# Optimization experiments

Measured on AMD Instinct MI355X. Metric: run time of the kernel, lower is better.

Reference implementation:

```python
import jax, jax.numpy as jnp
import numpy as np

N, D, H, G = 4096, 256, 4, 16
HEAD_DIM = D // H
LN_EPS = 1e-5
TEMP = 5.0


def setup_inputs() -> dict:
    key = jax.random.key(0)
    ks = jax.random.split(key, 12)
    s = 0.05  # weight init scale
    nrm = lambda k, shp: jax.random.normal(k, shp, jnp.float32) * s
    return {
        "x": jax.random.normal(ks[0], (N, D), jnp.float32),
        "Wq": nrm(ks[1], (D, D)), "bq": jnp.zeros((D,), jnp.float32),
        "Wk": nrm(ks[2], (D, D)), "bk": jnp.zeros((D,), jnp.float32),
        "Wv": nrm(ks[3], (D, D)), "bv": jnp.zeros((D,), jnp.float32),
        "Wv1": nrm(ks[4], (D, D // 2)), "bv1": jnp.zeros((D // 2,), jnp.float32),
        "Wv2": nrm(ks[5], (D // 2, 1)), "bv2": jnp.zeros((1,), jnp.float32),
        "Wc1": nrm(ks[6], (2 * D, D)), "bc1": jnp.zeros((D,), jnp.float32),
        "Wc2": nrm(ks[7], (D, 1)), "bc2": jnp.zeros((1,), jnp.float32),
        "gamma": jnp.ones((D,), jnp.float32),
        "beta": jnp.zeros((D,), jnp.float32),
        "batch": jnp.sort(jax.random.randint(ks[8], (N,), 0, G)),
    }


def reference(x, Wq, bq, Wk, bk, Wv, bv, Wv1, bv1, Wv2, bv2,
              Wc1, bc1, Wc2, bc2, gamma, beta, batch):
    n = x.shape[0]
    # multi-head projections -> [N, H, head_dim]
    Q = (x @ Wq + bq).reshape(n, H, HEAD_DIM)
    K = (x @ Wk + bk).reshape(n, H, HEAD_DIM)
    V = (x @ Wv + bv).reshape(n, H, HEAD_DIM)

    # dense scores [N, N, H], block-diagonal mask by graph membership
    scores = jnp.einsum('nhd,mhd->nmh', Q, K) / np.sqrt(HEAD_DIM).astype(np.float32)
    same_graph = (batch[:, None] == batch[None, :])  # [N, N]
    scores = jnp.where(same_graph[:, :, None], scores, -jnp.inf)
    probs = jax.nn.softmax(scores, axis=1)  # softmax over keys m (dim=1, as in torch)
    # dropout is identity in eval mode
    attended = jnp.einsum('nmh,mhd->nhd', probs, V).reshape(n, D)

    # vulnerability detector MLP: D -> D/2 -> 1, sigmoid
    vuln = jax.nn.sigmoid(jax.nn.relu(x @ Wv1 + bv1) @ Wv2 + bv2)[:, 0]

    # global max pool per graph, broadcast back to nodes
    graph_ctx = jax.ops.segment_max(x, batch, num_segments=G, indices_are_sorted=True)[batch]
    combined = jnp.concatenate([x, graph_ctx], axis=1)  # [N, 2D]
    ctx = jax.nn.sigmoid(jnp.tanh(combined @ Wc1 + bc1) @ Wc2 + bc2)[:, 0]

    mha_avg = probs.mean(axis=(1, 2))  # [N]
    w = 0.6 * vuln + 0.3 * ctx + 0.1 * mha_avg

    # per-graph segment softmax with temperature 5.0
    w5 = w * TEMP
    seg_max = jax.ops.segment_max(w5, batch, num_segments=G, indices_are_sorted=True)[batch]
    e = jnp.exp(w5 - seg_max)
    seg_sum = jax.ops.segment_sum(e, batch, num_segments=G, indices_are_sorted=True)[batch]
    att = e / seg_sum  # [N]

    out = attended * att[:, None] + x  # residual
    # LayerNorm over last dim
    mu = out.mean(axis=-1, keepdims=True)
    var = out.var(axis=-1, keepdims=True)
    out = (out - mu) * jax.lax.rsqrt(var + LN_EPS) * gamma + beta
    return out, att
```

## Files before the change

kernel.cpp:

```cpp
#include <hip/hip_runtime.h>
#include <math.h>

#define N_NODES 4096
#define DIM 256
#define NH 4
#define NG 16
#define LN_EPS 1e-5f
#define TEMP 5.0f
#define RSLACK 4160
#define PS_STRIDE 72
#define QT_MAX 24
#define KC_MAX 6
#define WPG (KC_MAX * QT_MAX * NH)
#define ATTN_UNITS (NG * WPG / 4)

typedef __attribute__((ext_vector_type(8))) short short8;
typedef __attribute__((ext_vector_type(4))) short short4_t;
typedef __attribute__((ext_vector_type(4))) float f32x4;

__device__ __forceinline__ unsigned short f2bf(float f) {
    unsigned u = __builtin_bit_cast(unsigned, f);
    u += 0x7FFFu + ((u >> 16) & 1u);
    return (unsigned short)(u >> 16);
}
__device__ __forceinline__ float bf2f(unsigned short u) {
    return __builtin_bit_cast(float, (unsigned)u << 16);
}
__device__ __forceinline__ float fsigmoid(float z) { return 1.f / (1.f + __expf(-z)); }
__device__ __forceinline__ float ftanh(float z) {
    float t = __expf(2.f * z);
    return (t - 1.f) / (t + 1.f);
}
__device__ __forceinline__ int seg_search(const int* __restrict__ batch, int g) {
    int lo = 0, hi = N_NODES;
    while (lo < hi) {
        int mid = (lo + hi) >> 1;
        if (batch[mid] < g) lo = mid + 1; else hi = mid;
    }
    return lo;
}

__global__ __launch_bounds__(256) void prep_kernel(
    const float* __restrict__ x, const float* __restrict__ Wq,
    const float* __restrict__ Wk, const float* __restrict__ Wv,
    const float* __restrict__ Wv1, const float* __restrict__ Wc1,
    const int* __restrict__ batch,
    unsigned short* __restrict__ xb, unsigned short* __restrict__ WqT,
    unsigned short* __restrict__ WkT, unsigned short* __restrict__ WvT,
    unsigned short* __restrict__ Wv1T, unsigned short* __restrict__ Wc1T,
    float* __restrict__ smax, int* __restrict__ seg) {
    int id = blockIdx.x, tid = threadIdx.x;
    if (id == 1632) {
        if (tid <= NG) seg[tid] = seg_search(batch, tid);
        return;
    }
    if (id >= 1376) {
        int u = id - 1376;
        int gg = u >> 4, c = u & 15;
        int s = seg_search(batch, gg), e = seg_search(batch, gg + 1);
        float mx = -INFINITY;
        for (int i = s + c; i < e; i += 16) mx = fmaxf(mx, x[(size_t)i * DIM + tid]);
        smax[(size_t)u * 256 + tid] = mx;
        return;
    }
    if (id >= 352) {
        int base = (id - 352) * 1024 + tid * 4;
        float4 v = *(const float4*)&x[base];
        short4_t o = {(short)f2bf(v.x), (short)f2bf(v.y), (short)f2bf(v.z), (short)f2bf(v.w)};
        *(short4_t*)&xb[base] = o;
        return;
    }
    const float* src; unsigned short* dst; int K, Nn, tX, rel;
    if (id < 64)       { src = Wq;  dst = WqT;  K = 256; Nn = 256; rel = id;      tX = 8;  }
    else if (id < 128) { src = Wk;  dst = WkT;  K = 256; Nn = 256; rel = id-64;   tX = 8;  }
    else if (id < 192) { src = Wv;  dst = WvT;  K = 256; Nn = 256; rel = id-128;  tX = 8;  }
    else if (id < 224) { src = Wv1; dst = Wv1T; K = 256; Nn = 128; rel = id-192;  tX = 8;  }
    else               { src = Wc1; dst = Wc1T; K = 512; Nn = 256; rel = id-224;  tX = 16; }
    int k0 = (rel % tX) * 32, n0 = (rel / tX) * 32;
    __shared__ float t[32][33];
    int c = tid & 31, r0 = tid >> 5;
#pragma unroll
    for (int p = 0; p < 4; ++p) {
        int rr = p * 8 + r0;
        t[rr][c] = src[(size_t)(k0 + rr) * Nn + n0 + c];
    }
    __syncthreads();
#pragma unroll
    for (int p = 0; p < 4; ++p) {
        int rr = p * 8 + r0;
        dst[(size_t)(n0 + rr) * K + k0 + c] = f2bf(t[c][rr]);
    }
}

__device__ __forceinline__ void gemm_unit(
    int z, int bx, int by,
    const unsigned short* __restrict__ xb,
    const unsigned short* __restrict__ WqT, const unsigned short* __restrict__ WkT,
    const unsigned short* __restrict__ WvT, const unsigned short* __restrict__ Wv1T,
    const unsigned short* __restrict__ Wc1T,
    const float* __restrict__ bq, const float* __restrict__ bk,
    const float* __restrict__ bv, const float* __restrict__ bv1,
    const float* __restrict__ bc1, const float* __restrict__ gcw,
    const float* __restrict__ Wv2, const float* __restrict__ Wc2,
    const int* __restrict__ batch,
    unsigned short* __restrict__ Qb, unsigned short* __restrict__ Kb,
    unsigned short* __restrict__ Vt, float* __restrict__ vacc,
    float* __restrict__ cacc) {
    const unsigned short* WT;
    const float* bias;
    int wstride = 256;
    switch (z) {
        case 0: WT = WqT; bias = bq; break;
        case 1: WT = WkT; bias = bk; break;
        case 2: WT = WvT; bias = bv; break;
        case 3: WT = Wc1T; bias = bc1; wstride = 512; break;
        default: WT = Wv1T; bias = bv1; break;
    }
    int ntn = (z == 4) ? 2 : 4;
    int nt0 = by * ntn;
    int tid = threadIdx.x;
    int w = tid >> 6, lane = tid & 63, m = lane & 15, quad = lane >> 4;
    int bm = bx * 64;
    int rowA = bm + 16 * w + m;
    short8 a[8];
#pragma unroll
    for (int ks = 0; ks < 8; ++ks)
        a[ks] = *(const short8*)&xb[(size_t)rowA * 256 + ks * 32 + quad * 8];
    int node0 = bm + 16 * w + quad * 4;
    int b4[4];
    if (z == 3) {
#pragma unroll
        for (int r = 0; r < 4; ++r) b4[r] = batch[node0 + r];
    }
    for (int nti = 0; nti < ntn; ++nti) {
        int nt = nt0 + nti;
        f32x4 acc = {0.f, 0.f, 0.f, 0.f};
#pragma unroll
        for (int ks = 0; ks < 8; ++ks) {
            short8 b = *(const short8*)&WT[(size_t)(nt * 16 + m) * wstride + ks * 32 + quad * 8];
            acc = __builtin_amdgcn_mfma_f32_16x16x32_bf16(a[ks], b, acc, 0, 0, 0);
        }
        int col = nt * 16 + m;
        float bb = bias[col];
        if (z == 0) {
#pragma unroll
            for (int r = 0; r < 4; ++r) Qb[(size_t)(node0 + r) * 256 + col] = f2bf(acc[r] + bb);
        } else if (z == 1) {
#pragma unroll
            for (int r = 0; r < 4; ++r) Kb[(size_t)(node0 + r) * 256 + col] = f2bf(acc[r] + bb);
        } else if (z == 2) {
            short4_t pk = {(short)f2bf(acc[0] + bb), (short)f2bf(acc[1] + bb),
                           (short)f2bf(acc[2] + bb), (short)f2bf(acc[3] + bb)};
            *(short4_t*)&Vt[(size_t)col * RSLACK + node0] = pk;
        } else if (z == 3) {
            float wc = Wc2[col];
#pragma unroll
            for (int r = 0; r < 4; ++r) {
                float p = ftanh(acc[r] + bb + gcw[b4[r] * 256 + col]) * wc;
#pragma unroll
                for (int mm = 1; mm < 16; mm <<= 1) p += __shfl_xor(p, mm);
                if (m == 0) atomicAdd(&cacc[node0 + r], p);
            }
        } else {
            float wv = Wv2[col];
#pragma unroll
            for (int r = 0; r < 4; ++r) {
                float p = fmaxf(acc[r] + bb, 0.f) * wv;
#pragma unroll
                for (int mm = 1; mm < 16; mm <<= 1) p += __shfl_xor(p, mm);
                if (m == 0) atomicAdd(&vacc[node0 + r], p);
            }
        }
    }
}

__global__ __launch_bounds__(256) void gemm_kernel(
    const unsigned short* __restrict__ xb, const float* __restrict__ smax,
    const float* __restrict__ Wc1,
    const unsigned short* __restrict__ WqT, const unsigned short* __restrict__ WkT,
    const unsigned short* __restrict__ WvT, const unsigned short* __restrict__ Wv1T,
    const unsigned short* __restrict__ Wc1T,
    const float* __restrict__ bq, const float* __restrict__ bk,
    const float* __restrict__ bv, const float* __restrict__ bv1,
    const float* __restrict__ bc1, const float* __restrict__ Wv2,
    const float* __restrict__ Wc2, const int* __restrict__ batch,
    unsigned short* __restrict__ Qb, unsigned short* __restrict__ Kb,
    unsigned short* __restrict__ Vt, float* __restrict__ vacc,
    float* __restrict__ gcw) {
    int tid = threadIdx.x;
    if (blockIdx.x < 16) {
        int g = blockIdx.x;
        __shared__ float gl[256];
        float mx = smax[(size_t)(g * 16) * 256 + tid];
#pragma unroll
        for (int c = 1; c < 16; ++c)
            mx = fmaxf(mx, smax[(size_t)(g * 16 + c) * 256 + tid]);
        gl[tid] = bf2f(f2bf(mx));
        __syncthreads();
        float a0 = 0.f, a1 = 0.f, a2 = 0.f, a3 = 0.f;
        for (int k = 0; k < 256; k += 4) {
            a0 += gl[k + 0] * Wc1[(size_t)(256 + k + 0) * 256 + tid];
            a1 += gl[k + 1] * Wc1[(size_t)(256 + k + 1) * 256 + tid];
            a2 += gl[k + 2] * Wc1[(size_t)(256 + k + 2) * 256 + tid];
            a3 += gl[k + 3] * Wc1[(size_t)(256 + k + 3) * 256 + tid];
        }
        gcw[g * 256 + tid] = (a0 + a1) + (a2 + a3);
        return;
    }
    int u = blockIdx.x - 16;
    int zi = u >> 8;
    int z = (zi == 3) ? 4 : zi;
    int r = u & 255;
    gemm_unit(z, r & 63, r >> 6, xb, WqT, WkT, WvT, Wv1T, Wc1T,
              bq, bk, bv, bv1, bc1, nullptr, Wv2, Wc2, batch,
              Qb, Kb, Vt, vacc, nullptr);
}

__global__ __launch_bounds__(256) void attn_kernel(
    const unsigned short* __restrict__ xb,
    const unsigned short* __restrict__ Qb, const unsigned short* __restrict__ Kb,
    const unsigned short* __restrict__ Vt, const int* __restrict__ seg,
    const unsigned short* __restrict__ Wc1T, const float* __restrict__ bc1,
    const float* __restrict__ gcw, const float* __restrict__ Wc2,
    const int* __restrict__ batch,
    unsigned short* __restrict__ Opart, float* __restrict__ Lpart,
    float* __restrict__ cacc) {
    int tid = threadIdx.x;
    if (blockIdx.x < 256) {
        int r = blockIdx.x;
        gemm_unit(3, r & 63, r >> 6, xb, nullptr, nullptr, nullptr, nullptr, Wc1T,
                  nullptr, nullptr, nullptr, nullptr, bc1, gcw, nullptr, Wc2, batch,
                  nullptr, nullptr, nullptr, nullptr, cacc);
        return;
    }
    __shared__ unsigned short Ps[4 * 16 * PS_STRIDE];
    int w = tid >> 6, lane = tid & 63, m = lane & 15, quad = lane >> 4;
    int wid = (blockIdx.x - 256) * 4 + w;
    int g = wid / WPG;
    int r1 = wid - g * WPG;
    int kc = r1 / (QT_MAX * NH);
    int r2 = r1 - kc * (QT_MAX * NH);
    int qt = r2 >> 2, h = r2 & 3;
    int s = seg[g], e = seg[g + 1];
    int q0 = s + qt * 16;
    int k0 = s + kc * 64;
    if (q0 >= e || k0 >= e) return;

    short8 qa0 = *(const short8*)&Qb[(size_t)(q0 + m) * 256 + h * 64 + quad * 8];
    short8 qa1 = *(const short8*)&Qb[(size_t)(q0 + m) * 256 + h * 64 + 32 + quad * 8];

    f32x4 S[4];
#pragma unroll
    for (int nt = 0; nt < 4; ++nt) {
        int key = k0 + nt * 16 + m;
        short8 kb0 = *(const short8*)&Kb[(size_t)key * 256 + h * 64 + quad * 8];
        short8 kb1 = *(const short8*)&Kb[(size_t)key * 256 + h * 64 + 32 + quad * 8];
        f32x4 sa = {0.f, 0.f, 0.f, 0.f};
        sa = __builtin_amdgcn_mfma_f32_16x16x32_bf16(qa0, kb0, sa, 0, 0, 0);
        sa = __builtin_amdgcn_mfma_f32_16x16x32_bf16(qa1, kb1, sa, 0, 0, 0);
        S[nt] = sa;
    }
    int wbase = w * 16 * PS_STRIDE;
#pragma unroll
    for (int nt = 0; nt < 4; ++nt) {
        bool valid = (k0 + nt * 16 + m) < e;
#pragma unroll
        for (int r = 0; r < 4; ++r) {
            float p = valid ? __expf(S[nt][r] * 0.125f) : 0.f;
            Ps[wbase + (quad * 4 + r) * PS_STRIDE + nt * 16 + m] = f2bf(p);
        }
    }
    __builtin_amdgcn_wave_barrier();
    short8 pa0 = *(const short8*)&Ps[wbase + m * PS_STRIDE + quad * 8];
    short8 pa1 = *(const short8*)&Ps[wbase + m * PS_STRIDE + 32 + quad * 8];

    short8 ones = {16256, 16256, 16256, 16256, 16256, 16256, 16256, 16256};
    f32x4 Lacc = {0.f, 0.f, 0.f, 0.f};
    Lacc = __builtin_amdgcn_mfma_f32_16x16x32_bf16(pa0, ones, Lacc, 0, 0, 0);
    Lacc = __builtin_amdgcn_mfma_f32_16x16x32_bf16(pa1, ones, Lacc, 0, 0, 0);
    f32x4 O[4];
#pragma unroll
    for (int nt = 0; nt < 4; ++nt) {
        const unsigned short* vrow = &Vt[(size_t)(h * 64 + nt * 16 + m) * RSLACK + k0];
        short8 vb0 = *(const short8*)&vrow[quad * 8];
        short8 vb1 = *(const short8*)&vrow[32 + quad * 8];
        f32x4 oa = {0.f, 0.f, 0.f, 0.f};
        oa = __builtin_amdgcn_mfma_f32_16x16x32_bf16(pa0, vb0, oa, 0, 0, 0);
        oa = __builtin_amdgcn_mfma_f32_16x16x32_bf16(pa1, vb1, oa, 0, 0, 0);
        O[nt] = oa;
    }
#pragma unroll
    for (int r = 0; r < 4; ++r) {
        int q = q0 + quad * 4 + r;
        if (q < e) {
            if (m == 0) Lpart[((size_t)kc * N_NODES + q) * 4 + h] = Lacc[r];
#pragma unroll
            for (int nt = 0; nt < 4; ++nt)
                Opart[((size_t)kc * N_NODES + q) * 256 + h * 64 + nt * 16 + m] =
                    f2bf(O[nt][r]);
        }
    }
}

__global__ __launch_bounds__(256) void final_kernel(
    const unsigned short* __restrict__ Opart, const float* __restrict__ Lpart,
    const float* __restrict__ x, const float* __restrict__ vacc,
    const float* __restrict__ cacc, const float* __restrict__ bv2,
    const float* __restrict__ bc2, const float* __restrict__ gamma,
    const float* __restrict__ beta, const int* __restrict__ batch,
    const int* __restrict__ seg, float* __restrict__ out,
    float* __restrict__ att_out) {
    int n = blockIdx.x;
    int tid = threadIdx.x;
    int g = batch[n];
    int s = seg[g], e = seg[g + 1];
    float vb = bv2[0], cb = bc2[0];
    __shared__ float r1[4], r2[4];
    int i1 = s + tid, i2 = s + 256 + tid;
    float w1 = (i1 < e) ? TEMP * (0.6f * fsigmoid(vacc[i1] + vb) +
                                  0.3f * fsigmoid(cacc[i1] + cb) + 0.1f / 4096.f)
                        : -1e30f;
    float w2 = (i2 < e) ? TEMP * (0.6f * fsigmoid(vacc[i2] + vb) +
                                  0.3f * fsigmoid(cacc[i2] + cb) + 0.1f / 4096.f)
                        : -1e30f;
    float mx = fmaxf(w1, w2);
#pragma unroll
    for (int k2 = 32; k2; k2 >>= 1) mx = fmaxf(mx, __shfl_xor(mx, k2));
    if ((tid & 63) == 0) r1[tid >> 6] = mx;
    __syncthreads();
    float m = fmaxf(fmaxf(r1[0], r1[1]), fmaxf(r1[2], r1[3]));
    float sm = ((i1 < e) ? __expf(w1 - m) : 0.f) + ((i2 < e) ? __expf(w2 - m) : 0.f);
#pragma unroll
    for (int k2 = 32; k2; k2 >>= 1) sm += __shfl_xor(sm, k2);
    __syncthreads();
    if ((tid & 63) == 0) r2[tid >> 6] = sm;
    __syncthreads();
    float ssum = r2[0] + r2[1] + r2[2] + r2[3];
    float w5n = TEMP * (0.6f * fsigmoid(vacc[n] + vb) + 0.3f * fsigmoid(cacc[n] + cb) +
                        0.1f / 4096.f);
    float att_n = __expf(w5n - m) / ssum;
    if (tid == 0) att_out[n] = att_n;
    int h = tid >> 6;
    float L = 0.f, O = 0.f;
#pragma unroll
    for (int c = 0; c < KC_MAX; ++c) {
        bool valid = (s + c * 64) < e;
        float lv = Lpart[((size_t)c * N_NODES + n) * 4 + h];
        float ov = bf2f(Opart[((size_t)c * N_NODES + n) * 256 + tid]);
        if (valid) { L += lv; O += ov; }
    }
    float o = (O / L) * att_n + x[(size_t)n * 256 + tid];
    float s1 = o, s2 = o * o;
#pragma unroll
    for (int k2 = 32; k2; k2 >>= 1) {
        s1 += __shfl_xor(s1, k2);
        s2 += __shfl_xor(s2, k2);
    }
    __syncthreads();
    if ((tid & 63) == 0) { r1[tid >> 6] = s1; r2[tid >> 6] = s2; }
    __syncthreads();
    float mu = (r1[0] + r1[1] + r1[2] + r1[3]) * (1.f / 256.f);
    float ms = (r2[0] + r2[1] + r2[2] + r2[3]) * (1.f / 256.f);
    float rs = rsqrtf(ms - mu * mu + LN_EPS);
    out[(size_t)n * 256 + tid] = (o - mu) * rs * gamma[tid] + beta[tid];
}

extern "C" void kernel_launch(void* const* d_in, const int* in_sizes, int n_in,
                              void* d_out, int out_size, void* d_ws, size_t ws_size,
                              hipStream_t stream) {
    const float* x     = (const float*)d_in[0];
    const float* Wq    = (const float*)d_in[1];
    const float* bq    = (const float*)d_in[2];
    const float* Wk    = (const float*)d_in[3];
    const float* bk    = (const float*)d_in[4];
    const float* Wv    = (const float*)d_in[5];
    const float* bv    = (const float*)d_in[6];
    const float* Wv1   = (const float*)d_in[7];
    const float* bv1   = (const float*)d_in[8];
    const float* Wv2   = (const float*)d_in[9];
    const float* bv2   = (const float*)d_in[10];
    const float* Wc1   = (const float*)d_in[11];
    const float* bc1   = (const float*)d_in[12];
    const float* Wc2   = (const float*)d_in[13];
    const float* bc2   = (const float*)d_in[14];
    const float* gamma = (const float*)d_in[15];
    const float* beta  = (const float*)d_in[16];
    const int*   batch = (const int*)d_in[17];

    float* out = (float*)d_out;
    float* att = out + N_NODES * DIM;

    float* vacc  = (float*)d_ws;
    float* cacc  = vacc + N_NODES;
    float* smax  = cacc + N_NODES;
    float* Lpart = smax + 256 * 256;
    float* gcw   = Lpart + KC_MAX * N_NODES * 4;
    int*   seg   = (int*)(gcw + NG * DIM);
    unsigned short* bws   = (unsigned short*)(seg + 32);
    unsigned short* xb    = bws;
    unsigned short* Qb    = xb + N_NODES * DIM;
    unsigned short* Kb    = Qb + RSLACK * DIM;
    unsigned short* Vt    = Kb + RSLACK * DIM;
    unsigned short* WqT   = Vt + DIM * RSLACK;
    unsigned short* WkT   = WqT + DIM * DIM;
    unsigned short* WvT   = WkT + DIM * DIM;
    unsigned short* Wv1T  = WvT + DIM * DIM;
    unsigned short* Wc1T  = Wv1T + 128 * DIM;
    unsigned short* Opart = Wc1T + DIM * 512;

    hipMemsetAsync(d_ws, 0, 2 * N_NODES * sizeof(float), stream);
    prep_kernel<<<1633, 256, 0, stream>>>(x, Wq, Wk, Wv, Wv1, Wc1, batch,
                                          xb, WqT, WkT, WvT, Wv1T, Wc1T, smax, seg);
    gemm_kernel<<<1040, 256, 0, stream>>>(xb, smax, Wc1, WqT, WkT, WvT, Wv1T, Wc1T,
                                          bq, bk, bv, bv1, bc1, Wv2, Wc2, batch,
                                          Qb, Kb, Vt, vacc, gcw);
    attn_kernel<<<ATTN_UNITS + 256, 256, 0, stream>>>(xb, Qb, Kb, Vt, seg, Wc1T, bc1,
                                                      gcw, Wc2, batch,
                                                      Opart, Lpart, cacc);
    final_kernel<<<N_NODES, 256, 0, stream>>>(Opart, Lpart, x, vacc, cacc, bv2, bc2,
                                              gamma, beta, batch, seg, out, att);
}
```

Measured before the change: 167.7 us.

## Fuse prep into GEMMs, drop memset and atomics, batch final kernel by 8 nodes

Removes the separate prep kernel and memset. The GEMM kernels now convert x and the weights to bf16 on the fly, staging transposed weight tiles in LDS, and compute the segment max pooling in-kernel. Atomic accumulation of the MLP head outputs is replaced by per-tile partial sums that the final kernel reduces. The 1/sqrt(d) scale is folded into Q, and the final kernel handles 8 nodes per block with a per-graph softmax computed once in shared memory. In exchange, each GEMM block repeats the weight conversion and the Wc1 GEMM uses smaller column tiles.

```diff
diff --git a/kernel.cpp b/kernel.cpp
--- a/kernel.cpp
+++ b/kernel.cpp
@@ -9,6 +9,7 @@
 #define TEMP 5.0f
 #define RSLACK 4160
 #define PS_STRIDE 72
+#define BS_STRIDE 264
 #define QT_MAX 24
 #define KC_MAX 6
 #define WPG (KC_MAX * QT_MAX * NH)
@@ -40,162 +41,66 @@
     return lo;
 }
 
-__global__ __launch_bounds__(256) void prep_kernel(
-    const float* __restrict__ x, const float* __restrict__ Wq,
-    const float* __restrict__ Wk, const float* __restrict__ Wv,
-    const float* __restrict__ Wv1, const float* __restrict__ Wc1,
-    const int* __restrict__ batch,
-    unsigned short* __restrict__ xb, unsigned short* __restrict__ WqT,
-    unsigned short* __restrict__ WkT, unsigned short* __restrict__ WvT,
-    unsigned short* __restrict__ Wv1T, unsigned short* __restrict__ Wc1T,
-    float* __restrict__ smax, int* __restrict__ seg) {
-    int id = blockIdx.x, tid = threadIdx.x;
-    if (id == 1632) {
-        if (tid <= NG) seg[tid] = seg_search(batch, tid);
-        return;
-    }
-    if (id >= 1376) {
-        int u = id - 1376;
-        int gg = u >> 4, c = u & 15;
-        int s = seg_search(batch, gg), e = seg_search(batch, gg + 1);
-        float mx = -INFINITY;
-        for (int i = s + c; i < e; i += 16) mx = fmaxf(mx, x[(size_t)i * DIM + tid]);
-        smax[(size_t)u * 256 + tid] = mx;
-        return;
-    }
-    if (id >= 352) {
-        int base = (id - 352) * 1024 + tid * 4;
-        float4 v = *(const float4*)&x[base];
-        short4_t o = {(short)f2bf(v.x), (short)f2bf(v.y), (short)f2bf(v.z), (short)f2bf(v.w)};
-        *(short4_t*)&xb[base] = o;
-        return;
-    }
-    const float* src; unsigned short* dst; int K, Nn, tX, rel;
-    if (id < 64)       { src = Wq;  dst = WqT;  K = 256; Nn = 256; rel = id;      tX = 8;  }
-    else if (id < 128) { src = Wk;  dst = WkT;  K = 256; Nn = 256; rel = id-64;   tX = 8;  }
-    else if (id < 192) { src = Wv;  dst = WvT;  K = 256; Nn = 256; rel = id-128;  tX = 8;  }
-    else if (id < 224) { src = Wv1; dst = Wv1T; K = 256; Nn = 128; rel = id-192;  tX = 8;  }
-    else               { src = Wc1; dst = Wc1T; K = 512; Nn = 256; rel = id-224;  tX = 16; }
-    int k0 = (rel % tX) * 32, n0 = (rel / tX) * 32;
-    __shared__ float t[32][33];
-    int c = tid & 31, r0 = tid >> 5;
-#pragma unroll
-    for (int p = 0; p < 4; ++p) {
-        int rr = p * 8 + r0;
-        t[rr][c] = src[(size_t)(k0 + rr) * Nn + n0 + c];
+__device__ __forceinline__ short8 afrag_f32(const float* __restrict__ x, int row, int k0) {
+    float4 a = *(const float4*)&x[(size_t)row * 256 + k0];
+    float4 b = *(const float4*)&x[(size_t)row * 256 + k0 + 4];
+    short8 r = {(short)f2bf(a.x), (short)f2bf(a.y), (short)f2bf(a.z), (short)f2bf(a.w),
+                (short)f2bf(b.x), (short)f2bf(b.y), (short)f2bf(b.z), (short)f2bf(b.w)};
+    return r;
+}
+
+__device__ __forceinline__ void ldsB(const float* __restrict__ W, int ws, int bn,
+                                     int ncols, unsigned short* __restrict__ Bs) {
+    int tpr = ncols >> 2;
+    int c4 = (threadIdx.x & (tpr - 1)) * 4;
+    int r0 = threadIdx.x / tpr;
+    int rpp = 256 / tpr;
+    for (int p = 0; p < (ncols >> 2); ++p) {
+        int k = p * rpp + r0;
+        float4 wv = *(const float4*)&W[(size_t)k * ws + bn + c4];
+        Bs[(c4 + 0) * BS_STRIDE + k] = f2bf(wv.x);
+        Bs[(c4 + 1) * BS_STRIDE + k] = f2bf(wv.y);
+        Bs[(c4 + 2) * BS_STRIDE + k] = f2bf(wv.z);
+        Bs[(c4 + 3) * BS_STRIDE + k] = f2bf(wv.w);
     }
     __syncthreads();
-#pragma unroll
-    for (int p = 0; p < 4; ++p) {
-        int rr = p * 8 + r0;
-        dst[(size_t)(n0 + rr) * K + k0 + c] = f2bf(t[c][rr]);
-    }
-}
-
-__device__ __forceinline__ void gemm_unit(
-    int z, int bx, int by,
-    const unsigned short* __restrict__ xb,
-    const unsigned short* __restrict__ WqT, const unsigned short* __restrict__ WkT,
-    const unsigned short* __restrict__ WvT, const unsigned short* __restrict__ Wv1T,
-    const unsigned short* __restrict__ Wc1T,
-    const float* __restrict__ bq, const float* __restrict__ bk,
-    const float* __restrict__ bv, const float* __restrict__ bv1,
-    const float* __restrict__ bc1, const float* __restrict__ gcw,
-    const float* __restrict__ Wv2, const float* __restrict__ Wc2,
+}
+
+__global__ __launch_bounds__(256) void k1_kernel(
+    const float* __restrict__ x,
+    const float* __restrict__ Wq, const float* __restrict__ bq,
+    const float* __restrict__ Wk, const float* __restrict__ bk,
+    const float* __restrict__ Wv, const float* __restrict__ bv,
+    const float* __restrict__ Wv1, const float* __restrict__ bv1,
+    const float* __restrict__ Wv2, const float* __restrict__ Wc1,
     const int* __restrict__ batch,
     unsigned short* __restrict__ Qb, unsigned short* __restrict__ Kb,
-    unsigned short* __restrict__ Vt, float* __restrict__ vacc,
-    float* __restrict__ cacc) {
-    const unsigned short* WT;
-    const float* bias;
-    int wstride = 256;
-    switch (z) {
-        case 0: WT = WqT; bias = bq; break;
-        case 1: WT = WkT; bias = bk; break;
-        case 2: WT = WvT; bias = bv; break;
-        case 3: WT = Wc1T; bias = bc1; wstride = 512; break;
-        default: WT = Wv1T; bias = bv1; break;
-    }
-    int ntn = (z == 4) ? 2 : 4;
-    int nt0 = by * ntn;
-    int tid = threadIdx.x;
-    int w = tid >> 6, lane = tid & 63, m = lane & 15, quad = lane >> 4;
-    int bm = bx * 64;
-    int rowA = bm + 16 * w + m;
-    short8 a[8];
-#pragma unroll
-    for (int ks = 0; ks < 8; ++ks)
-        a[ks] = *(const short8*)&xb[(size_t)rowA * 256 + ks * 32 + quad * 8];
-    int node0 = bm + 16 * w + quad * 4;
-    int b4[4];
-    if (z == 3) {
-#pragma unroll
-        for (int r = 0; r < 4; ++r) b4[r] = batch[node0 + r];
-    }
-    for (int nti = 0; nti < ntn; ++nti) {
-        int nt = nt0 + nti;
-        f32x4 acc = {0.f, 0.f, 0.f, 0.f};
-#pragma unroll
-        for (int ks = 0; ks < 8; ++ks) {
-            short8 b = *(const short8*)&WT[(size_t)(nt * 16 + m) * wstride + ks * 32 + quad * 8];
-            acc = __builtin_amdgcn_mfma_f32_16x16x32_bf16(a[ks], b, acc, 0, 0, 0);
-        }
-        int col = nt * 16 + m;
-        float bb = bias[col];
-        if (z == 0) {
-#pragma unroll
-            for (int r = 0; r < 4; ++r) Qb[(size_t)(node0 + r) * 256 + col] = f2bf(acc[r] + bb);
-        } else if (z == 1) {
-#pragma unroll
-            for (int r = 0; r < 4; ++r) Kb[(size_t)(node0 + r) * 256 + col] = f2bf(acc[r] + bb);
-        } else if (z == 2) {
-            short4_t pk = {(short)f2bf(acc[0] + bb), (short)f2bf(acc[1] + bb),
-                           (short)f2bf(acc[2] + bb), (short)f2bf(acc[3] + bb)};
-            *(short4_t*)&Vt[(size_t)col * RSLACK + node0] = pk;
-        } else if (z == 3) {
-            float wc = Wc2[col];
-#pragma unroll
-            for (int r = 0; r < 4; ++r) {
-                float p = ftanh(acc[r] + bb + gcw[b4[r] * 256 + col]) * wc;
-#pragma unroll
-                for (int mm = 1; mm < 16; mm <<= 1) p += __shfl_xor(p, mm);
-                if (m == 0) atomicAdd(&cacc[node0 + r], p);
+    unsigned short* __restrict__ Vt, float* __restrict__ vacc2,
+    float* __restrict__ gcw, int* __restrict__ seg) {
+    __shared__ __align__(16) char smem[64 * BS_STRIDE * 2];
+    int id = blockIdx.x, tid = threadIdx.x;
+    if (id < 16) {
+        int g = id;
+        int s = seg_search(batch, g), e = seg_search(batch, g + 1);
+        float* red = (float*)smem;
+        float* gl  = (float*)smem + 1024;
+        int c4 = (tid & 63) * 4, way = tid >> 6;
+        float4 mx = {-INFINITY, -INFINITY, -INFINITY, -INFINITY};
+        for (int i = s + way; i < e; i += 4) {
+            float4 v = *(const float4*)&x[(size_t)i * DIM + c4];
+            mx.x = fmaxf(mx.x, v.x); mx.y = fmaxf(mx.y, v.y);
+            mx.z = fmaxf(mx.z, v.z); mx.w = fmaxf(mx.w, v.w);
+        }
+        *(float4*)&red[way * 256 + c4] = mx;
+        __syncthreads();
+        if (way == 0) {
+#pragma unroll
+            for (int j = 0; j < 4; ++j) {
+                float mm = fmaxf(fmaxf(red[c4 + j], red[256 + c4 + j]),
+                                 fmaxf(red[512 + c4 + j], red[768 + c4 + j]));
+                gl[c4 + j] = bf2f(f2bf(mm));
             }
-        } else {
-            float wv = Wv2[col];
-#pragma unroll
-            for (int r = 0; r < 4; ++r) {
-                float p = fmaxf(acc[r] + bb, 0.f) * wv;
-#pragma unroll
-                for (int mm = 1; mm < 16; mm <<= 1) p += __shfl_xor(p, mm);
-                if (m == 0) atomicAdd(&vacc[node0 + r], p);
-            }
-        }
-    }
-}
-
-__global__ __launch_bounds__(256) void gemm_kernel(
-    const unsigned short* __restrict__ xb, const float* __restrict__ smax,
-    const float* __restrict__ Wc1,
-    const unsigned short* __restrict__ WqT, const unsigned short* __restrict__ WkT,
-    const unsigned short* __restrict__ WvT, const unsigned short* __restrict__ Wv1T,
-    const unsigned short* __restrict__ Wc1T,
-    const float* __restrict__ bq, const float* __restrict__ bk,
-    const float* __restrict__ bv, const float* __restrict__ bv1,
-    const float* __restrict__ bc1, const float* __restrict__ Wv2,
-    const float* __restrict__ Wc2, const int* __restrict__ batch,
-    unsigned short* __restrict__ Qb, unsigned short* __restrict__ Kb,
-    unsigned short* __restrict__ Vt, float* __restrict__ vacc,
-    float* __restrict__ gcw) {
-    int tid = threadIdx.x;
-    if (blockIdx.x < 16) {
-        int g = blockIdx.x;
-        __shared__ float gl[256];
-        float mx = smax[(size_t)(g * 16) * 256 + tid];
-#pragma unroll
-        for (int c = 1; c < 16; ++c)
-            mx = fmaxf(mx, smax[(size_t)(g * 16 + c) * 256 + tid]);
-        gl[tid] = bf2f(f2bf(mx));
+        }
         __syncthreads();
         float a0 = 0.f, a1 = 0.f, a2 = 0.f, a3 = 0.f;
         for (int k = 0; k < 256; k += 4) {
@@ -207,40 +112,125 @@
         gcw[g * 256 + tid] = (a0 + a1) + (a2 + a3);
         return;
     }
-    int u = blockIdx.x - 16;
-    int zi = u >> 8;
-    int z = (zi == 3) ? 4 : zi;
-    int r = u & 255;
-    gemm_unit(z, r & 63, r >> 6, xb, WqT, WkT, WvT, Wv1T, Wc1T,
-              bq, bk, bv, bv1, bc1, nullptr, Wv2, Wc2, batch,
-              Qb, Kb, Vt, vacc, nullptr);
-}
-
-__global__ __launch_bounds__(256) void attn_kernel(
-    const unsigned short* __restrict__ xb,
+    if (id == 16) {
+        if (tid <= NG) seg[tid] = seg_search(batch, tid);
+        return;
+    }
+    int u = id - 17;
+    unsigned short* Bs = (unsigned short*)smem;
+    int w = tid >> 6, lane = tid & 63, m = lane & 15, quad = lane >> 4;
+    if (u < 768) {
+        int z = u >> 8, r = u & 255, bx = r & 63, by = r >> 6;
+        const float* W = (z == 0) ? Wq : (z == 1) ? Wk : Wv;
+        const float* bias = (z == 0) ? bq : (z == 1) ? bk : bv;
+        ldsB(W, 256, by * 64, 64, Bs);
+        int rowA = bx * 64 + 16 * w + m;
+        short8 a[8];
+#pragma unroll
+        for (int ks = 0; ks < 8; ++ks) a[ks] = afrag_f32(x, rowA, ks * 32 + quad * 8);
+        int node0 = bx * 64 + 16 * w + quad * 4;
+#pragma unroll
+        for (int nt = 0; nt < 4; ++nt) {
+            f32x4 acc = {0.f, 0.f, 0.f, 0.f};
+#pragma unroll
+            for (int ks = 0; ks < 8; ++ks) {
+                short8 b = *(const short8*)&Bs[(nt * 16 + m) * BS_STRIDE + ks * 32 + quad * 8];
+                acc = __builtin_amdgcn_mfma_f32_16x16x32_bf16(a[ks], b, acc, 0, 0, 0);
+            }
+            int col = by * 64 + nt * 16 + m;
+            float bb = bias[col];
+            if (z == 0) {
+#pragma unroll
+                for (int r2 = 0; r2 < 4; ++r2)
+                    Qb[(size_t)(node0 + r2) * 256 + col] = f2bf((acc[r2] + bb) * 0.125f);
+            } else if (z == 1) {
+#pragma unroll
+                for (int r2 = 0; r2 < 4; ++r2)
+                    Kb[(size_t)(node0 + r2) * 256 + col] = f2bf(acc[r2] + bb);
+            } else {
+                short4_t pk = {(short)f2bf(acc[0] + bb), (short)f2bf(acc[1] + bb),
+                               (short)f2bf(acc[2] + bb), (short)f2bf(acc[3] + bb)};
+                *(short4_t*)&Vt[(size_t)col * RSLACK + node0] = pk;
+            }
+        }
+    } else {
+        int r = u - 768, bx = r & 63, by = r >> 6;
+        ldsB(Wv1, 128, by * 64, 64, Bs);
+        int rowA = bx * 64 + 16 * w + m;
+        short8 a[8];
+#pragma unroll
+        for (int ks = 0; ks < 8; ++ks) a[ks] = afrag_f32(x, rowA, ks * 32 + quad * 8);
+        int node0 = bx * 64 + 16 * w + quad * 4;
+        float psum[4] = {0.f, 0.f, 0.f, 0.f};
+#pragma unroll
+        for (int nt = 0; nt < 4; ++nt) {
+            f32x4 acc = {0.f, 0.f, 0.f, 0.f};
+#pragma unroll
+            for (int ks = 0; ks < 8; ++ks) {
+                short8 b = *(const short8*)&Bs[(nt * 16 + m) * BS_STRIDE + ks * 32 + quad * 8];
+                acc = __builtin_amdgcn_mfma_f32_16x16x32_bf16(a[ks], b, acc, 0, 0, 0);
+            }
+            int col = by * 64 + nt * 16 + m;
+            float bb = bv1[col], wv = Wv2[col];
+#pragma unroll
+            for (int r2 = 0; r2 < 4; ++r2) psum[r2] += fmaxf(acc[r2] + bb, 0.f) * wv;
+        }
+#pragma unroll
+        for (int r2 = 0; r2 < 4; ++r2) {
+#pragma unroll
+            for (int mm = 1; mm < 16; mm <<= 1) psum[r2] += __shfl_xor(psum[r2], mm);
+            if (m == 0) vacc2[(size_t)(node0 + r2) * 2 + by] = psum[r2];
+        }
+    }
+}
+
+__global__ __launch_bounds__(256) void k2_kernel(
+    const float* __restrict__ x, const float* __restrict__ Wc1,
+    const float* __restrict__ bc1, const float* __restrict__ Wc2,
+    const float* __restrict__ gcw, const int* __restrict__ batch,
     const unsigned short* __restrict__ Qb, const unsigned short* __restrict__ Kb,
     const unsigned short* __restrict__ Vt, const int* __restrict__ seg,
-    const unsigned short* __restrict__ Wc1T, const float* __restrict__ bc1,
-    const float* __restrict__ gcw, const float* __restrict__ Wc2,
-    const int* __restrict__ batch,
     unsigned short* __restrict__ Opart, float* __restrict__ Lpart,
-    float* __restrict__ cacc) {
+    float* __restrict__ cacc16) {
+    __shared__ __align__(16) char smem[9216];
     int tid = threadIdx.x;
-    if (blockIdx.x < 256) {
-        int r = blockIdx.x;
-        gemm_unit(3, r & 63, r >> 6, xb, nullptr, nullptr, nullptr, nullptr, Wc1T,
-                  nullptr, nullptr, nullptr, nullptr, bc1, gcw, nullptr, Wc2, batch,
-                  nullptr, nullptr, nullptr, nullptr, cacc);
+    int w = tid >> 6, lane = tid & 63, m = lane & 15, quad = lane >> 4;
+    if (blockIdx.x < 1024) {
+        int bx = blockIdx.x & 63, by = blockIdx.x >> 6;
+        unsigned short* Bs = (unsigned short*)smem;
+        ldsB(Wc1, 256, by * 16, 16, Bs);
+        int rowA = bx * 64 + 16 * w + m;
+        short8 a[8];
+#pragma unroll
+        for (int ks = 0; ks < 8; ++ks) a[ks] = afrag_f32(x, rowA, ks * 32 + quad * 8);
+        int node0 = bx * 64 + 16 * w + quad * 4;
+        int b4[4];
+#pragma unroll
+        for (int r2 = 0; r2 < 4; ++r2) b4[r2] = batch[node0 + r2];
+        f32x4 acc = {0.f, 0.f, 0.f, 0.f};
+#pragma unroll
+        for (int ks = 0; ks < 8; ++ks) {
+            short8 b = *(const short8*)&Bs[m * BS_STRIDE + ks * 32 + quad * 8];
+            acc = __builtin_amdgcn_mfma_f32_16x16x32_bf16(a[ks], b, acc, 0, 0, 0);
+        }
+        int col = by * 16 + m;
+        float bb = bc1[col], wc = Wc2[col];
+#pragma unroll
+        for (int r2 = 0; r2 < 4; ++r2) {
+            float p = ftanh(acc[r2] + bb + gcw[b4[r2] * 256 + col]) * wc;
+#pragma unroll
+            for (int mm = 1; mm < 16; mm <<= 1) p += __shfl_xor(p, mm);
+            if (m == 0) cacc16[(size_t)(node0 + r2) * 16 + by] = p;
+        }
         return;
     }
-    __shared__ unsigned short Ps[4 * 16 * PS_STRIDE];
-    int w = tid >> 6, lane = tid & 63, m = lane & 15, quad = lane >> 4;
-    int wid = (blockIdx.x - 256) * 4 + w;
+    unsigned short* Ps = (unsigned short*)smem;
+    int wid = (blockIdx.x - 1024) * 4 + w;
     int g = wid / WPG;
     int r1 = wid - g * WPG;
     int kc = r1 / (QT_MAX * NH);
-    int r2 = r1 - kc * (QT_MAX * NH);
-    int qt = r2 >> 2, h = r2 & 3;
+    int r2i = r1 - kc * (QT_MAX * NH);
+    int qt = r2i >> 2, h = r2i & 3;
     int s = seg[g], e = seg[g + 1];
     int q0 = s + qt * 16;
     int k0 = s + kc * 64;
@@ -265,9 +255,9 @@
     for (int nt = 0; nt < 4; ++nt) {
         bool valid = (k0 + nt * 16 + m) < e;
 #pragma unroll
-        for (int r = 0; r < 4; ++r) {
-            float p = valid ? __expf(S[nt][r] * 0.125f) : 0.f;
-            Ps[wbase + (quad * 4 + r) * PS_STRIDE + nt * 16 + m] = f2bf(p);
+        for (int r3 = 0; r3 < 4; ++r3) {
+            float p = valid ? __expf(S[nt][r3]) : 0.f;
+            Ps[wbase + (quad * 4 + r3) * PS_STRIDE + nt * 16 + m] = f2bf(p);
         }
     }
     __builtin_amdgcn_wave_barrier();
@@ -290,79 +280,98 @@
         O[nt] = oa;
     }
 #pragma unroll
-    for (int r = 0; r < 4; ++r) {
-        int q = q0 + quad * 4 + r;
+    for (int r3 = 0; r3 < 4; ++r3) {
+        int q = q0 + quad * 4 + r3;
         if (q < e) {
-            if (m == 0) Lpart[((size_t)kc * N_NODES + q) * 4 + h] = Lacc[r];
+            if (m == 0) Lpart[((size_t)kc * N_NODES + q) * 4 + h] = Lacc[r3];
 #pragma unroll
             for (int nt = 0; nt < 4; ++nt)
                 Opart[((size_t)kc * N_NODES + q) * 256 + h * 64 + nt * 16 + m] =
-                    f2bf(O[nt][r]);
-        }
-    }
-}
-
-__global__ __launch_bounds__(256) void final_kernel(
+                    f2bf(O[nt][r3]);
+        }
+    }
+}
+
+__global__ __launch_bounds__(256) void k3_kernel(
     const unsigned short* __restrict__ Opart, const float* __restrict__ Lpart,
-    const float* __restrict__ x, const float* __restrict__ vacc,
-    const float* __restrict__ cacc, const float* __restrict__ bv2,
+    const float* __restrict__ x, const float* __restrict__ vacc2,
+    const float* __restrict__ cacc16, const float* __restrict__ bv2,
     const float* __restrict__ bc2, const float* __restrict__ gamma,
     const float* __restrict__ beta, const int* __restrict__ batch,
     const int* __restrict__ seg, float* __restrict__ out,
     float* __restrict__ att_out) {
-    int n = blockIdx.x;
+    __shared__ float wsc[776];
+    __shared__ float gm[8], gsum[8];
+    __shared__ float r1[4], r2[4];
     int tid = threadIdx.x;
-    int g = batch[n];
-    int s = seg[g], e = seg[g + 1];
+    int n0 = blockIdx.x * 8;
+    int gf = batch[n0], gl = batch[n0 + 7];
+    int s0 = seg[gf], e1 = seg[gl + 1];
     float vb = bv2[0], cb = bc2[0];
-    __shared__ float r1[4], r2[4];
-    int i1 = s + tid, i2 = s + 256 + tid;
-    float w1 = (i1 < e) ? TEMP * (0.6f * fsigmoid(vacc[i1] + vb) +
-                                  0.3f * fsigmoid(cacc[i1] + cb) + 0.1f / 4096.f)
-                        : -1e30f;
-    float w2 = (i2 < e) ? TEMP * (0.6f * fsigmoid(vacc[i2] + vb) +
-                                  0.3f * fsigmoid(cacc[i2] + cb) + 0.1f / 4096.f)
-                        : -1e30f;
-    float mx = fmaxf(w1, w2);
-#pragma unroll
-    for (int k2 = 32; k2; k2 >>= 1) mx = fmaxf(mx, __shfl_xor(mx, k2));
-    if ((tid & 63) == 0) r1[tid >> 6] = mx;
+    for (int j = s0 + tid; j < e1; j += 256) {
+        float2 vv = *(const float2*)&vacc2[(size_t)j * 2];
+        float4 c0 = *(const float4*)&cacc16[(size_t)j * 16];
+        float4 c1 = *(const float4*)&cacc16[(size_t)j * 16 + 4];
+        float4 c2 = *(const float4*)&cacc16[(size_t)j * 16 + 8];
+        float4 c3 = *(const float4*)&cacc16[(size_t)j * 16 + 12];
+        float cs = ((c0.x + c0.y) + (c0.z + c0.w)) + ((c1.x + c1.y) + (c1.z + c1.w)) +
+                   ((c2.x + c2.y) + (c2.z + c2.w)) + ((c3.x + c3.y) + (c3.z + c3.w));
+        wsc[j - s0] = TEMP * (0.6f * fsigmoid(vv.x + vv.y + vb) +
+                              0.3f * fsigmoid(cs + cb) + 0.1f / 4096.f);
+    }
     __syncthreads();
-    float m = fmaxf(fmaxf(r1[0], r1[1]), fmaxf(r1[2], r1[3]));
-    float sm = ((i1 < e) ? __expf(w1 - m) : 0.f) + ((i2 < e) ? __expf(w2 - m) : 0.f);
-#pragma unroll
-    for (int k2 = 32; k2; k2 >>= 1) sm += __shfl_xor(sm, k2);
-    __syncthreads();
-    if ((tid & 63) == 0) r2[tid >> 6] = sm;
-    __syncthreads();
-    float ssum = r2[0] + r2[1] + r2[2] + r2[3];
-    float w5n = TEMP * (0.6f * fsigmoid(vacc[n] + vb) + 0.3f * fsigmoid(cacc[n] + cb) +
-                        0.1f / 4096.f);
-    float att_n = __expf(w5n - m) / ssum;
-    if (tid == 0) att_out[n] = att_n;
-    int h = tid >> 6;
-    float L = 0.f, O = 0.f;
-#pragma unroll
-    for (int c = 0; c < KC_MAX; ++c) {
-        bool valid = (s + c * 64) < e;
-        float lv = Lpart[((size_t)c * N_NODES + n) * 4 + h];
-        float ov = bf2f(Opart[((size_t)c * N_NODES + n) * 256 + tid]);
-        if (valid) { L += lv; O += ov; }
-    }
-    float o = (O / L) * att_n + x[(size_t)n * 256 + tid];
-    float s1 = o, s2 = o * o;
-#pragma unroll
-    for (int k2 = 32; k2; k2 >>= 1) {
-        s1 += __shfl_xor(s1, k2);
-        s2 += __shfl_xor(s2, k2);
-    }
-    __syncthreads();
-    if ((tid & 63) == 0) { r1[tid >> 6] = s1; r2[tid >> 6] = s2; }
-    __syncthreads();
-    float mu = (r1[0] + r1[1] + r1[2] + r1[3]) * (1.f / 256.f);
-    float ms = (r2[0] + r2[1] + r2[2] + r2[3]) * (1.f / 256.f);
-    float rs = rsqrtf(ms - mu * mu + LN_EPS);
-    out[(size_t)n * 256 + tid] = (o - mu) * rs * gamma[tid] + beta[tid];
+    for (int g = gf; g <= gl; ++g) {
+        int gs_ = seg[g], ge = seg[g + 1];
+        float mx = -1e30f;
+        for (int j = gs_ + tid; j < ge; j += 256) mx = fmaxf(mx, wsc[j - s0]);
+#pragma unroll
+        for (int k2 = 32; k2; k2 >>= 1) mx = fmaxf(mx, __shfl_xor(mx, k2));
+        if ((tid & 63) == 0) r1[tid >> 6] = mx;
+        __syncthreads();
+        mx = fmaxf(fmaxf(r1[0], r1[1]), fmaxf(r1[2], r1[3]));
+        float sm = 0.f;
+        for (int j = gs_ + tid; j < ge; j += 256) sm += __expf(wsc[j - s0] - mx);
+#pragma unroll
+        for (int k2 = 32; k2; k2 >>= 1) sm += __shfl_xor(sm, k2);
+        __syncthreads();
+        if ((tid & 63) == 0) r2[tid >> 6] = sm;
+        __syncthreads();
+        if (tid == 0) {
+            gm[g - gf] = mx;
+            gsum[g - gf] = r2[0] + r2[1] + r2[2] + r2[3];
+        }
+        __syncthreads();
+    }
+    for (int i = 0; i < 8; ++i) {
+        int n = n0 + i;
+        int g = batch[n];
+        int s = seg[g], e = seg[g + 1];
+        float att_n = __expf(wsc[n - s0] - gm[g - gf]) / gsum[g - gf];
+        if (tid == 0) att_out[n] = att_n;
+        int h = tid >> 6;
+        float L = 0.f, O = 0.f;
+#pragma unroll
+        for (int c = 0; c < KC_MAX; ++c) {
+            bool valid = (s + c * 64) < e;
+            float lv = Lpart[((size_t)c * N_NODES + n) * 4 + h];
+            float ov = bf2f(Opart[((size_t)c * N_NODES + n) * 256 + tid]);
+            if (valid) { L += lv; O += ov; }
+        }
+        float o = (O / L) * att_n + x[(size_t)n * 256 + tid];
+        float s1 = o, s2 = o * o;
+#pragma unroll
+        for (int k2 = 32; k2; k2 >>= 1) {
+            s1 += __shfl_xor(s1, k2);
+            s2 += __shfl_xor(s2, k2);
+        }
+        __syncthreads();
+        if ((tid & 63) == 0) { r1[tid >> 6] = s1; r2[tid >> 6] = s2; }
+        __syncthreads();
+        float mu = (r1[0] + r1[1] + r1[2] + r1[3]) * (1.f / 256.f);
+        float ms = (r2[0] + r2[1] + r2[2] + r2[3]) * (1.f / 256.f);
+        float rs = rsqrtf(ms - mu * mu + LN_EPS);
+        out[(size_t)n * 256 + tid] = (o - mu) * rs * gamma[tid] + beta[tid];
+    }
 }
 
 extern "C" void kernel_launch(void* const* d_in, const int* in_sizes, int n_in,
@@ -390,33 +399,22 @@
     float* out = (float*)d_out;
     float* att = out + N_NODES * DIM;
 
-    float* vacc  = (float*)d_ws;
-    float* cacc  = vacc + N_NODES;
-    float* smax  = cacc + N_NODES;
-    float* Lpart = smax + 256 * 256;
-    float* gcw   = Lpart + KC_MAX * N_NODES * 4;
-    int*   seg   = (int*)(gcw + NG * DIM);
-    unsigned short* bws   = (unsigned short*)(seg + 32);
-    unsigned short* xb    = bws;
-    unsigned short* Qb    = xb + N_NODES * DIM;
+    float* vacc2  = (float*)d_ws;
+    float* cacc16 = vacc2 + N_NODES * 2;
+    float* gcw    = cacc16 + N_NODES * 16;
+    float* Lpart  = gcw + NG * DIM;
+    int*   seg    = (int*)(Lpart + KC_MAX * N_NODES * 4);
+    unsigned short* Qb    = (unsigned short*)(seg + 32);
     unsigned short* Kb    = Qb + RSLACK * DIM;
     unsigned short* Vt    = Kb + RSLACK * DIM;
-    unsigned short* WqT   = Vt + DIM * RSLACK;
-    unsigned short* WkT   = WqT + DIM * DIM;
-    unsigned short* WvT   = WkT + DIM * DIM;
-    unsigned short* Wv1T  = WvT + DIM * DIM;
-    unsigned short* Wc1T  = Wv1T + 128 * DIM;
-    unsigned short* Opart = Wc1T + DIM * 512;
-
-    hipMemsetAsync(d_ws, 0, 2 * N_NODES * sizeof(float), stream);
-    prep_kernel<<<1633, 256, 0, stream>>>(x, Wq, Wk, Wv, Wv1, Wc1, batch,
-                                          xb, WqT, WkT, WvT, Wv1T, Wc1T, smax, seg);
-    gemm_kernel<<<1040, 256, 0, stream>>>(xb, smax, Wc1, WqT, WkT, WvT, Wv1T, Wc1T,
-                                          bq, bk, bv, bv1, bc1, Wv2, Wc2, batch,
-                                          Qb, Kb, Vt, vacc, gcw);
-    attn_kernel<<<ATTN_UNITS + 256, 256, 0, stream>>>(xb, Qb, Kb, Vt, seg, Wc1T, bc1,
-                                                      gcw, Wc2, batch,
-                                                      Opart, Lpart, cacc);
-    final_kernel<<<N_NODES, 256, 0, stream>>>(Opart, Lpart, x, vacc, cacc, bv2, bc2,
-                                              gamma, beta, batch, seg, out, att);
-}
+    unsigned short* Opart = Vt + DIM * RSLACK;
+
+    k1_kernel<<<913, 256, 0, stream>>>(x, Wq, bq, Wk, bk, Wv, bv, Wv1, bv1, Wv2,
+                                       Wc1, batch, Qb, Kb, Vt, vacc2, gcw, seg);
+    k2_kernel<<<1024 + ATTN_UNITS, 256, 0, stream>>>(x, Wc1, bc1, Wc2, gcw, batch,
+                                                     Qb, Kb, Vt, seg,
+                                                     Opart, Lpart, cacc16);
+    k3_kernel<<<N_NODES / 8, 256, 0, stream>>>(Opart, Lpart, x, vacc2, cacc16,
+                                               bv2, bc2, gamma, beta, batch, seg,
+                                               out, att);
+}
```

Result: slower. 174.1 us (+3.8%).
